# Performance work log

Measured on AMD Instinct MI355X. Metric: run time of the kernel, lower is better.

## Reference

```python
import jax, jax.numpy as jnp
import numpy as np

SMOOTH = 1e-05
N_SCALES = 3
# 3x3 cross-shaped boundary kernel, OIHW layout [1,1,3,3]
_KERNEL = jnp.array([[0., 1., 0.], [1., 1., 1.], [0., 1., 0.]], jnp.float32).reshape(1, 1, 3, 3)


def _nearest_ds(t, h, w):
    """torch F.interpolate mode='nearest': src_idx = floor(dst_idx * in/out)."""
    H, W = t.shape[-2], t.shape[-1]
    ih = (jnp.arange(h) * H) // h
    iw = (jnp.arange(w) * W) // w
    return t[..., ih[:, None], iw[None, :]]


def _boundary_dou(probs, tgt, valid):
    # probs, tgt: [B,N,h,w] float32; valid: [B,N] float32 in {0,1}
    B, N, h, w = probs.shape
    Y = jax.lax.conv_general_dilated(
        tgt.reshape(B * N, 1, h, w), _KERNEL,
        window_strides=(1, 1), padding=[(1, 1), (1, 1)],
        dimension_numbers=('NCHW', 'OIHW', 'NCHW')).reshape(B, N, h, w)
    Y = Y * tgt
    Y = jnp.where(Y == 5.0, 0.0, Y)  # interior pixels zeroed, boundary kept
    C = jnp.sum(Y != 0, axis=(-2, -1)).astype(jnp.float32)   # [B,N] boundary count
    S = jnp.sum(tgt != 0, axis=(-2, -1)).astype(jnp.float32)  # [B,N] fg count
    alpha = 2.0 * (1.0 - (C + SMOOTH) / (S + SMOOTH)) - 1.0
    alpha = jnp.minimum(alpha, 0.8)
    inter = jnp.sum(probs * tgt, axis=(-2, -1))
    y_sum = jnp.sum(tgt * tgt, axis=(-2, -1))
    z_sum = jnp.sum(probs * probs, axis=(-2, -1))
    dou = (z_sum + y_sum - 2.0 * inter + SMOOTH) / (z_sum + y_sum - (1.0 + alpha) * inter + SMOOTH)
    per = jnp.where(S > 0, dou, probs.mean(axis=(-2, -1)))  # empty-target fallback
    cnt = valid.sum()
    return jnp.where(cnt > 0, (per * valid).sum() / cnt, 0.0)


def reference(logits0, logits1, logits2, targets, valid_mask):
    outs = [logits0, logits1, logits2]
    ws = np.array([1.0 / 2.0 ** i for i in range(N_SCALES)])
    ws = ws / ws.sum()  # nnU-Net deep supervision weights
    tgt_full = targets.astype(jnp.float32)
    valid = (valid_mask >= 0.5).astype(jnp.float32)
    loss = jnp.float32(0.0)
    for w_i, out in zip(ws, outs):
        h, w = out.shape[-2], out.shape[-1]
        tgt = _nearest_ds(tgt_full, h, w)
        probs = jax.nn.sigmoid(out.astype(jnp.float32))
        loss = loss + jnp.float32(w_i) * _boundary_dou(probs, tgt, valid)
    return loss


def setup_inputs() -> dict:
    key = jax.random.key(0)
    k0, k1, k2, kt = jax.random.split(key, 4)
    B, N = 8, 4
    return {
        'logits0': jax.random.normal(k0, (B, N, 512, 512), jnp.float32),
        'logits1': jax.random.normal(k1, (B, N, 256, 256), jnp.float32),
        'logits2': jax.random.normal(k2, (B, N, 128, 128), jnp.float32),
        'targets': jax.random.randint(kt, (B, N, 512, 512), 0, 2, jnp.int32),
        'valid_mask': jnp.ones((B, N), jnp.float32),
    }
```

## Files before the change

### kernel.cpp

```cpp
#include <hip/hip_runtime.h>

#define SMOOTH 1e-5f

typedef float floatx4 __attribute__((ext_vector_type(4)));
typedef float floatx2 __attribute__((ext_vector_type(2)));


__device__ __forceinline__ float wave_reduce(float v) {
#pragma unroll
    for (int off = 32; off; off >>= 1) v += __shfl_down(v, off, 64);
    return v;
}

__device__ __forceinline__ float sigmoidf(float x) {
    return 1.f / (1.f + __expf(-x));
}

__device__ __forceinline__ unsigned pack8(int4 a, int4 b) {
    return (unsigned)(a.x != 0)        | ((unsigned)(a.y != 0) << 1) |
           ((unsigned)(a.z != 0) << 2) | ((unsigned)(a.w != 0) << 3) |
           ((unsigned)(b.x != 0) << 4) | ((unsigned)(b.y != 0) << 5) |
           ((unsigned)(b.z != 0) << 6) | ((unsigned)(b.w != 0) << 7);
}
__device__ __forceinline__ unsigned pack4(int4 a, int4 b) {
    return (unsigned)(a.x != 0)        | ((unsigned)(a.z != 0) << 1) |
           ((unsigned)(b.x != 0) << 2) | ((unsigned)(b.z != 0) << 3);
}
__device__ __forceinline__ unsigned pack2(int a, int b) {
    return (unsigned)(a != 0) | ((unsigned)(b != 0) << 1);
}

template<int W>
__device__ __forceinline__ void row_proc(unsigned u, unsigned c, unsigned d,
    const float* pr, int lane, int& cC, int& cS, float& aI, float& aZ, float& aP)
{
    unsigned pv = __shfl_up(c, 1);
    unsigned nx = __shfl_down(c, 1);
    if (lane == 0)  pv = 0;
    if (lane == 63) nx = 0;
    const unsigned M = (1u << W) - 1u;
    unsigned lv = ((c << 1) | ((pv >> (W - 1)) & 1u)) & M;
    unsigned rv = ((c >> 1) | ((nx & 1u) << (W - 1))) & M;
    unsigned inter = c & u & d & lv & rv;
    cS += __popc(c);
    cC += __popc(c & ~inter);
#pragma unroll
    for (int j = 0; j < W; ++j) {
        float pj = pr[j];
        aI += ((c >> j) & 1u) ? pj : 0.f;
        aZ += pj * pj;
        aP += pj;
    }
}

__global__ __launch_bounds__(64) void bdou_reduce(
    const float* __restrict__ l0, const float* __restrict__ l1,
    const float* __restrict__ l2, const int* __restrict__ tgt,
    float* __restrict__ ws)
{
    const int blk  = blockIdx.x;
    const int lane = threadIdx.x;

    int scale, img, strip;
    if (blk < 1024)      { scale = 0; img = blk >> 5; strip = blk & 31; }
    else if (blk < 1536) { int b = blk - 1024; scale = 1; img = b >> 4; strip = b & 15; }
    else                 { int b = blk - 1536; scale = 2; img = b >> 3; strip = b & 7; }

    const int* __restrict__ timg = tgt + (size_t)img * 262144;
    const int y0 = strip * 16;

    int   cC = 0, cS = 0;
    float aI = 0.f, aZ = 0.f, aP = 0.f;

    if (scale == 0) {
        const int*   T = timg + lane * 8;
        const float* L = l0 + (size_t)img * 262144 + lane * 8;
        unsigned b_prev, b_cur, b_next;
        floatx4 lgA, lgB;
        {
            int yp = (y0 > 0) ? y0 - 1 : 0;
            int4 a0 = *(const int4*)(T + (size_t)yp * 512);
            int4 a1 = *(const int4*)(T + (size_t)yp * 512 + 4);
            int4 c0 = *(const int4*)(T + (size_t)y0 * 512);
            int4 c1 = *(const int4*)(T + (size_t)y0 * 512 + 4);
            int4 d0 = *(const int4*)(T + (size_t)(y0 + 1) * 512);
            int4 d1 = *(const int4*)(T + (size_t)(y0 + 1) * 512 + 4);
            lgA = *(const floatx4*)(L + (size_t)y0 * 512);
            lgB = *(const floatx4*)(L + (size_t)y0 * 512 + 4);
            b_prev = pack8(a0, a1); b_cur = pack8(c0, c1); b_next = pack8(d0, d1);
        }
        for (int i = 0; i < 16; ++i) {
            int y   = y0 + i;
            int ypf = (y + 2 < 512) ? y + 2 : 511;
            int ylg = (y + 1 < 512) ? y + 1 : 511;
            int4 p0 = *(const int4*)(T + (size_t)ypf * 512);
            int4 p1 = *(const int4*)(T + (size_t)ypf * 512 + 4);
            floatx4 nA = *(const floatx4*)(L + (size_t)ylg * 512);
            floatx4 nB = *(const floatx4*)(L + (size_t)ylg * 512 + 4);
            unsigned u = (y > 0)   ? b_prev : 0u;
            unsigned d = (y < 511) ? b_next : 0u;
            float pr[8] = {sigmoidf(lgA.x), sigmoidf(lgA.y), sigmoidf(lgA.z), sigmoidf(lgA.w),
                           sigmoidf(lgB.x), sigmoidf(lgB.y), sigmoidf(lgB.z), sigmoidf(lgB.w)};
            row_proc<8>(u, b_cur, d, pr, lane, cC, cS, aI, aZ, aP);
            b_prev = b_cur; b_cur = b_next; b_next = pack8(p0, p1);
            lgA = nA; lgB = nB;
        }
    } else if (scale == 1) {
        const int*   T = timg + lane * 8;
        const float* L = l1 + (size_t)img * 65536 + lane * 4;
        unsigned b_prev, b_cur, b_next;
        floatx4 lgA;
        {
            int yp = (y0 > 0) ? y0 - 1 : 0;
            int4 a0 = *(const int4*)(T + (size_t)(2 * yp) * 512);
            int4 a1 = *(const int4*)(T + (size_t)(2 * yp) * 512 + 4);
            int4 c0 = *(const int4*)(T + (size_t)(2 * y0) * 512);
            int4 c1 = *(const int4*)(T + (size_t)(2 * y0) * 512 + 4);
            int4 d0 = *(const int4*)(T + (size_t)(2 * (y0 + 1)) * 512);
            int4 d1 = *(const int4*)(T + (size_t)(2 * (y0 + 1)) * 512 + 4);
            lgA = *(const floatx4*)(L + (size_t)y0 * 256);
            b_prev = pack4(a0, a1); b_cur = pack4(c0, c1); b_next = pack4(d0, d1);
        }
        for (int i = 0; i < 16; ++i) {
            int y   = y0 + i;
            int ypf = (y + 2 < 256) ? y + 2 : 255;
            int ylg = (y + 1 < 256) ? y + 1 : 255;
            int4 p0 = *(const int4*)(T + (size_t)(2 * ypf) * 512);
            int4 p1 = *(const int4*)(T + (size_t)(2 * ypf) * 512 + 4);
            floatx4 nA = *(const floatx4*)(L + (size_t)ylg * 256);
            unsigned u = (y > 0)   ? b_prev : 0u;
            unsigned d = (y < 255) ? b_next : 0u;
            float pr[4] = {sigmoidf(lgA.x), sigmoidf(lgA.y), sigmoidf(lgA.z), sigmoidf(lgA.w)};
            row_proc<4>(u, b_cur, d, pr, lane, cC, cS, aI, aZ, aP);
            b_prev = b_cur; b_cur = b_next; b_next = pack4(p0, p1);
            lgA = nA;
        }
    } else {
        const int*   T = timg + lane * 8;
        const float* L = l2 + (size_t)img * 16384 + lane * 2;
        unsigned b_prev, b_cur, b_next;
        floatx2 lgA;
        {
            int yp = (y0 > 0) ? y0 - 1 : 0;
            int a0 = T[(size_t)(4 * yp) * 512],       a1 = T[(size_t)(4 * yp) * 512 + 4];
            int c0 = T[(size_t)(4 * y0) * 512],       c1 = T[(size_t)(4 * y0) * 512 + 4];
            int d0 = T[(size_t)(4 * (y0 + 1)) * 512], d1 = T[(size_t)(4 * (y0 + 1)) * 512 + 4];
            lgA = *(const floatx2*)(L + (size_t)y0 * 128);
            b_prev = pack2(a0, a1); b_cur = pack2(c0, c1); b_next = pack2(d0, d1);
        }
        for (int i = 0; i < 16; ++i) {
            int y   = y0 + i;
            int ypf = (y + 2 < 128) ? y + 2 : 127;
            int ylg = (y + 1 < 128) ? y + 1 : 127;
            int p0 = T[(size_t)(4 * ypf) * 512];
            int p1 = T[(size_t)(4 * ypf) * 512 + 4];
            floatx2 nA = *(const floatx2*)(L + (size_t)ylg * 128);
            unsigned u = (y > 0)   ? b_prev : 0u;
            unsigned d = (y < 127) ? b_next : 0u;
            float pr[2] = {sigmoidf(lgA.x), sigmoidf(lgA.y)};
            row_proc<2>(u, b_cur, d, pr, lane, cC, cS, aI, aZ, aP);
            b_prev = b_cur; b_cur = b_next; b_next = pack2(p0, p1);
            lgA = nA;
        }
    }

    float vals[5] = {(float)cC, (float)cS, aI, aZ, aP};
#pragma unroll
    for (int k = 0; k < 5; ++k) vals[k] = wave_reduce(vals[k]);
    if (lane == 0) {
        float* w = ws + (scale * 32 + img) * 5;
        atomicAdd(&w[0], vals[0]);
        atomicAdd(&w[1], vals[1]);
        atomicAdd(&w[2], vals[2]);
        atomicAdd(&w[3], vals[3]);
        atomicAdd(&w[4], vals[4]);
    }
}

__global__ void bdou_final(const float* __restrict__ ws,
                           const float* __restrict__ valid_mask,
                           float* __restrict__ out)
{
    int tid = threadIdx.x;
    float contrib = 0.f, cpart = 0.f;
    if (tid < 96) {
        int s = tid >> 5, i = tid & 31;
        const float* w = ws + tid * 5;
        float C = w[0], S = w[1], I = w[2], Z = w[3], P = w[4];
        float valid = (valid_mask[i] >= 0.5f) ? 1.f : 0.f;
        float alpha = fminf(2.f * (1.f - (C + SMOOTH) / (S + SMOOTH)) - 1.f, 0.8f);
        float dou = (Z + S - 2.f * I + SMOOTH) /
                    (Z + S - (1.f + alpha) * I + SMOOTH);
        const float wts[3]  = {4.f / 7.f, 2.f / 7.f, 1.f / 7.f};
        const float pixc[3] = {262144.f, 65536.f, 16384.f};
        float per = (S > 0.f) ? dou : (P / pixc[s]);
        contrib = wts[s] * per * valid;
        if (tid < 32) cpart = valid;
    }
    contrib = wave_reduce(contrib);
    cpart   = wave_reduce(cpart);
    __shared__ float sm[2][2];
    int wv = tid >> 6, ln = tid & 63;
    if (ln == 0) { sm[wv][0] = contrib; sm[wv][1] = cpart; }
    __syncthreads();
    if (tid == 0) {
        float tot = sm[0][0] + sm[1][0];
        float cnt = sm[0][1] + sm[1][1];
        out[0] = (cnt > 0.f) ? tot / cnt : 0.f;
    }
}

extern "C" void kernel_launch(void* const* d_in, const int* in_sizes, int n_in,
                              void* d_out, int out_size, void* d_ws, size_t ws_size,
                              hipStream_t stream) {
    const float* l0 = (const float*)d_in[0];
    const float* l1 = (const float*)d_in[1];
    const float* l2 = (const float*)d_in[2];
    const int*   tg = (const int*)d_in[3];
    const float* vm = (const float*)d_in[4];
    float* ws = (float*)d_ws;

    (void)hipMemsetAsync(ws, 0, 3 * 32 * 5 * sizeof(float), stream);
    bdou_reduce<<<1792, 64, 0, stream>>>(l0, l1, l2, tg, ws);
    bdou_final<<<1, 128, 0, stream>>>(ws, vm, (float*)d_out);
}
```

Baseline: 125.6 us.

## Split boundary stencil from elementwise reductions into separate block roles

The single fused kernel is split into two kinds of work inside one launch. Most blocks (256 threads each) do flat, vectorized passes over logits and downsampled targets to accumulate foreground count, intersection, squared sum and probability sum. A set of extra blocks runs only the bitpacked cross-stencil boundary count, using two waves per block over 32-row strips. The intent is to raise parallelism and simplify the heavy per-pixel sigmoid path, at the cost of reading the target rows a second time and leaving half the threads idle in the stencil blocks.

```diff
diff --git a/kernel.cpp b/kernel.cpp
--- a/kernel.cpp
+++ b/kernel.cpp
@@ -3,7 +3,6 @@
 #define SMOOTH 1e-5f
 
 typedef float floatx4 __attribute__((ext_vector_type(4)));
-typedef float floatx2 __attribute__((ext_vector_type(2)));
 
 
 __device__ __forceinline__ float wave_reduce(float v) {
@@ -31,8 +30,7 @@
 }
 
 template<int W>
-__device__ __forceinline__ void row_proc(unsigned u, unsigned c, unsigned d,
-    const float* pr, int lane, int& cC, int& cS, float& aI, float& aZ, float& aP)
+__device__ __forceinline__ int stencil_cnt(unsigned u, unsigned c, unsigned d, int lane)
 {
     unsigned pv = __shfl_up(c, 1);
     unsigned nx = __shfl_down(c, 1);
@@ -41,139 +39,174 @@
     const unsigned M = (1u << W) - 1u;
     unsigned lv = ((c << 1) | ((pv >> (W - 1)) & 1u)) & M;
     unsigned rv = ((c >> 1) | ((nx & 1u) << (W - 1))) & M;
-    unsigned inter = c & u & d & lv & rv;
-    cS += __popc(c);
-    cC += __popc(c & ~inter);
-#pragma unroll
-    for (int j = 0; j < W; ++j) {
-        float pj = pr[j];
-        aI += ((c >> j) & 1u) ? pj : 0.f;
-        aZ += pj * pj;
-        aP += pj;
-    }
-}
-
-__global__ __launch_bounds__(64) void bdou_reduce(
+    return __popc(c & ~(u & d & lv & rv));
+}
+
+__global__ __launch_bounds__(256) void bdou_main(
     const float* __restrict__ l0, const float* __restrict__ l1,
     const float* __restrict__ l2, const int* __restrict__ tgt,
     float* __restrict__ ws)
 {
-    const int blk  = blockIdx.x;
-    const int lane = threadIdx.x;
-
-    int scale, img, strip;
-    if (blk < 1024)      { scale = 0; img = blk >> 5; strip = blk & 31; }
-    else if (blk < 1536) { int b = blk - 1024; scale = 1; img = b >> 4; strip = b & 15; }
-    else                 { int b = blk - 1536; scale = 2; img = b >> 3; strip = b & 7; }
-
-    const int* __restrict__ timg = tgt + (size_t)img * 262144;
-    const int y0 = strip * 16;
-
-    int   cC = 0, cS = 0;
-    float aI = 0.f, aZ = 0.f, aP = 0.f;
-
-    if (scale == 0) {
-        const int*   T = timg + lane * 8;
-        const float* L = l0 + (size_t)img * 262144 + lane * 8;
-        unsigned b_prev, b_cur, b_next;
-        floatx4 lgA, lgB;
-        {
-            int yp = (y0 > 0) ? y0 - 1 : 0;
-            int4 a0 = *(const int4*)(T + (size_t)yp * 512);
-            int4 a1 = *(const int4*)(T + (size_t)yp * 512 + 4);
-            int4 c0 = *(const int4*)(T + (size_t)y0 * 512);
-            int4 c1 = *(const int4*)(T + (size_t)y0 * 512 + 4);
-            int4 d0 = *(const int4*)(T + (size_t)(y0 + 1) * 512);
-            int4 d1 = *(const int4*)(T + (size_t)(y0 + 1) * 512 + 4);
-            lgA = *(const floatx4*)(L + (size_t)y0 * 512);
-            lgB = *(const floatx4*)(L + (size_t)y0 * 512 + 4);
-            b_prev = pack8(a0, a1); b_cur = pack8(c0, c1); b_next = pack8(d0, d1);
-        }
-        for (int i = 0; i < 16; ++i) {
-            int y   = y0 + i;
-            int ypf = (y + 2 < 512) ? y + 2 : 511;
-            int ylg = (y + 1 < 512) ? y + 1 : 511;
-            int4 p0 = *(const int4*)(T + (size_t)ypf * 512);
-            int4 p1 = *(const int4*)(T + (size_t)ypf * 512 + 4);
-            floatx4 nA = *(const floatx4*)(L + (size_t)ylg * 512);
-            floatx4 nB = *(const floatx4*)(L + (size_t)ylg * 512 + 4);
-            unsigned u = (y > 0)   ? b_prev : 0u;
-            unsigned d = (y < 511) ? b_next : 0u;
-            float pr[8] = {sigmoidf(lgA.x), sigmoidf(lgA.y), sigmoidf(lgA.z), sigmoidf(lgA.w),
-                           sigmoidf(lgB.x), sigmoidf(lgB.y), sigmoidf(lgB.z), sigmoidf(lgB.w)};
-            row_proc<8>(u, b_cur, d, pr, lane, cC, cS, aI, aZ, aP);
-            b_prev = b_cur; b_cur = b_next; b_next = pack8(p0, p1);
-            lgA = nA; lgB = nB;
-        }
-    } else if (scale == 1) {
-        const int*   T = timg + lane * 8;
-        const float* L = l1 + (size_t)img * 65536 + lane * 4;
-        unsigned b_prev, b_cur, b_next;
-        floatx4 lgA;
-        {
-            int yp = (y0 > 0) ? y0 - 1 : 0;
-            int4 a0 = *(const int4*)(T + (size_t)(2 * yp) * 512);
-            int4 a1 = *(const int4*)(T + (size_t)(2 * yp) * 512 + 4);
-            int4 c0 = *(const int4*)(T + (size_t)(2 * y0) * 512);
-            int4 c1 = *(const int4*)(T + (size_t)(2 * y0) * 512 + 4);
-            int4 d0 = *(const int4*)(T + (size_t)(2 * (y0 + 1)) * 512);
-            int4 d1 = *(const int4*)(T + (size_t)(2 * (y0 + 1)) * 512 + 4);
-            lgA = *(const floatx4*)(L + (size_t)y0 * 256);
-            b_prev = pack4(a0, a1); b_cur = pack4(c0, c1); b_next = pack4(d0, d1);
-        }
-        for (int i = 0; i < 16; ++i) {
-            int y   = y0 + i;
-            int ypf = (y + 2 < 256) ? y + 2 : 255;
-            int ylg = (y + 1 < 256) ? y + 1 : 255;
-            int4 p0 = *(const int4*)(T + (size_t)(2 * ypf) * 512);
-            int4 p1 = *(const int4*)(T + (size_t)(2 * ypf) * 512 + 4);
-            floatx4 nA = *(const floatx4*)(L + (size_t)ylg * 256);
-            unsigned u = (y > 0)   ? b_prev : 0u;
-            unsigned d = (y < 255) ? b_next : 0u;
-            float pr[4] = {sigmoidf(lgA.x), sigmoidf(lgA.y), sigmoidf(lgA.z), sigmoidf(lgA.w)};
-            row_proc<4>(u, b_cur, d, pr, lane, cC, cS, aI, aZ, aP);
-            b_prev = b_cur; b_cur = b_next; b_next = pack4(p0, p1);
-            lgA = nA;
+    const int blk = blockIdx.x;
+    const int tid = threadIdx.x;
+    const int w = tid >> 6, lane = tid & 63;
+
+    if (blk < 1344) {
+        int scale, img, chunk;
+        if (blk < 1024)      { scale = 0; img = blk >> 5; chunk = blk & 31; }
+        else if (blk < 1280) { int b = blk - 1024; scale = 1; img = b >> 3; chunk = b & 7; }
+        else                 { int b = blk - 1280; scale = 2; img = b >> 1; chunk = b & 1; }
+        const int* __restrict__ T = tgt + (size_t)img * 262144;
+        int cS = 0; float aI = 0.f, aZ = 0.f, aP = 0.f;
+        const int qbase = chunk * 2048 + tid;
+
+        if (scale == 0) {
+            const float* __restrict__ L = l0 + (size_t)img * 262144;
+#pragma unroll
+            for (int it = 0; it < 8; ++it) {
+                int p = (qbase + it * 256) * 4;
+                floatx4 lg = *(const floatx4*)(L + p);
+                int4    tv = *(const int4*)(T + p);
+                float pr[4] = {sigmoidf(lg.x), sigmoidf(lg.y), sigmoidf(lg.z), sigmoidf(lg.w)};
+                int   tb[4] = {tv.x != 0, tv.y != 0, tv.z != 0, tv.w != 0};
+#pragma unroll
+                for (int j = 0; j < 4; ++j) {
+                    cS += tb[j];
+                    aI += pr[j] * (float)tb[j];
+                    aZ += pr[j] * pr[j];
+                    aP += pr[j];
+                }
+            }
+        } else if (scale == 1) {
+            const float* __restrict__ L = l1 + (size_t)img * 65536;
+#pragma unroll
+            for (int it = 0; it < 8; ++it) {
+                int p = (qbase + it * 256) * 4;
+                int y = p >> 8, x = p & 255;
+                floatx4 lg = *(const floatx4*)(L + (size_t)y * 256 + x);
+                const int* r = T + (size_t)(2 * y) * 512 + 2 * x;
+                int4 a = *(const int4*)(r);
+                int4 b = *(const int4*)(r + 4);
+                float pr[4] = {sigmoidf(lg.x), sigmoidf(lg.y), sigmoidf(lg.z), sigmoidf(lg.w)};
+                int   tb[4] = {a.x != 0, a.z != 0, b.x != 0, b.z != 0};
+#pragma unroll
+                for (int j = 0; j < 4; ++j) {
+                    cS += tb[j];
+                    aI += pr[j] * (float)tb[j];
+                    aZ += pr[j] * pr[j];
+                    aP += pr[j];
+                }
+            }
+        } else {
+            const float* __restrict__ L = l2 + (size_t)img * 16384;
+#pragma unroll
+            for (int it = 0; it < 8; ++it) {
+                int p = (qbase + it * 256) * 4;
+                int y = p >> 7, x = p & 127;
+                floatx4 lg = *(const floatx4*)(L + (size_t)y * 128 + x);
+                const int* r = T + (size_t)(4 * y) * 512 + 4 * x;
+                int t0 = r[0], t1 = r[4], t2 = r[8], t3 = r[12];
+                float pr[4] = {sigmoidf(lg.x), sigmoidf(lg.y), sigmoidf(lg.z), sigmoidf(lg.w)};
+                int   tb[4] = {t0 != 0, t1 != 0, t2 != 0, t3 != 0};
+#pragma unroll
+                for (int j = 0; j < 4; ++j) {
+                    cS += tb[j];
+                    aI += pr[j] * (float)tb[j];
+                    aZ += pr[j] * pr[j];
+                    aP += pr[j];
+                }
+            }
+        }
+
+        __shared__ float red[4][4];
+        float vals[4] = {(float)cS, aI, aZ, aP};
+#pragma unroll
+        for (int k = 0; k < 4; ++k) vals[k] = wave_reduce(vals[k]);
+        if (lane == 0) {
+#pragma unroll
+            for (int k = 0; k < 4; ++k) red[w][k] = vals[k];
+        }
+        __syncthreads();
+        if (tid < 4) {
+            float s = red[0][tid] + red[1][tid] + red[2][tid] + red[3][tid];
+            atomicAdd(&ws[(scale * 32 + img) * 5 + 1 + tid], s);
         }
     } else {
-        const int*   T = timg + lane * 8;
-        const float* L = l2 + (size_t)img * 16384 + lane * 2;
-        unsigned b_prev, b_cur, b_next;
-        floatx2 lgA;
-        {
-            int yp = (y0 > 0) ? y0 - 1 : 0;
-            int a0 = T[(size_t)(4 * yp) * 512],       a1 = T[(size_t)(4 * yp) * 512 + 4];
-            int c0 = T[(size_t)(4 * y0) * 512],       c1 = T[(size_t)(4 * y0) * 512 + 4];
-            int d0 = T[(size_t)(4 * (y0 + 1)) * 512], d1 = T[(size_t)(4 * (y0 + 1)) * 512 + 4];
-            lgA = *(const floatx2*)(L + (size_t)y0 * 128);
-            b_prev = pack2(a0, a1); b_cur = pack2(c0, c1); b_next = pack2(d0, d1);
-        }
-        for (int i = 0; i < 16; ++i) {
-            int y   = y0 + i;
-            int ypf = (y + 2 < 128) ? y + 2 : 127;
-            int ylg = (y + 1 < 128) ? y + 1 : 127;
-            int p0 = T[(size_t)(4 * ypf) * 512];
-            int p1 = T[(size_t)(4 * ypf) * 512 + 4];
-            floatx2 nA = *(const floatx2*)(L + (size_t)ylg * 128);
-            unsigned u = (y > 0)   ? b_prev : 0u;
-            unsigned d = (y < 127) ? b_next : 0u;
-            float pr[2] = {sigmoidf(lgA.x), sigmoidf(lgA.y)};
-            row_proc<2>(u, b_cur, d, pr, lane, cC, cS, aI, aZ, aP);
-            b_prev = b_cur; b_cur = b_next; b_next = pack2(p0, p1);
-            lgA = nA;
-        }
-    }
-
-    float vals[5] = {(float)cC, (float)cS, aI, aZ, aP};
-#pragma unroll
-    for (int k = 0; k < 5; ++k) vals[k] = wave_reduce(vals[k]);
-    if (lane == 0) {
-        float* w = ws + (scale * 32 + img) * 5;
-        atomicAdd(&w[0], vals[0]);
-        atomicAdd(&w[1], vals[1]);
-        atomicAdd(&w[2], vals[2]);
-        atomicAdd(&w[3], vals[3]);
-        atomicAdd(&w[4], vals[4]);
+        if (w >= 2) return;
+        const int task = (blk - 1344) * 2 + w;
+        int scale, img, strip;
+        if (task < 512)      { scale = 0; img = task >> 4; strip = task & 15; }
+        else if (task < 768) { int b = task - 512; scale = 1; img = b >> 3; strip = b & 7; }
+        else                 { int b = task - 768; scale = 2; img = b >> 2; strip = b & 3; }
+        const int* __restrict__ T = tgt + (size_t)img * 262144 + lane * 8;
+        const int y0 = strip * 32;
+        int cC = 0;
+
+        if (scale == 0) {
+            unsigned rp = 0, rc;
+            if (y0 > 0) {
+                int4 a = *(const int4*)(T + (size_t)(y0 - 1) * 512);
+                int4 b = *(const int4*)(T + (size_t)(y0 - 1) * 512 + 4);
+                rp = pack8(a, b);
+            }
+            {
+                int4 a = *(const int4*)(T + (size_t)y0 * 512);
+                int4 b = *(const int4*)(T + (size_t)y0 * 512 + 4);
+                rc = pack8(a, b);
+            }
+            int4 f0 = *(const int4*)(T + (size_t)(y0 + 1) * 512);
+            int4 f1 = *(const int4*)(T + (size_t)(y0 + 1) * 512 + 4);
+            for (int i = 0; i < 32; ++i) {
+                int y = y0 + i;
+                unsigned rn = (y < 511) ? pack8(f0, f1) : 0u;
+                int yn = (y + 2 <= 511) ? y + 2 : 511;
+                f0 = *(const int4*)(T + (size_t)yn * 512);
+                f1 = *(const int4*)(T + (size_t)yn * 512 + 4);
+                cC += stencil_cnt<8>(rp, rc, rn, lane);
+                rp = rc; rc = rn;
+            }
+        } else if (scale == 1) {
+            unsigned rp = 0, rc;
+            if (y0 > 0) {
+                int4 a = *(const int4*)(T + (size_t)(2 * (y0 - 1)) * 512);
+                int4 b = *(const int4*)(T + (size_t)(2 * (y0 - 1)) * 512 + 4);
+                rp = pack4(a, b);
+            }
+            {
+                int4 a = *(const int4*)(T + (size_t)(2 * y0) * 512);
+                int4 b = *(const int4*)(T + (size_t)(2 * y0) * 512 + 4);
+                rc = pack4(a, b);
+            }
+            int4 f0 = *(const int4*)(T + (size_t)(2 * (y0 + 1)) * 512);
+            int4 f1 = *(const int4*)(T + (size_t)(2 * (y0 + 1)) * 512 + 4);
+            for (int i = 0; i < 32; ++i) {
+                int y = y0 + i;
+                unsigned rn = (y < 255) ? pack4(f0, f1) : 0u;
+                int yn = (y + 2 <= 255) ? y + 2 : 255;
+                f0 = *(const int4*)(T + (size_t)(2 * yn) * 512);
+                f1 = *(const int4*)(T + (size_t)(2 * yn) * 512 + 4);
+                cC += stencil_cnt<4>(rp, rc, rn, lane);
+                rp = rc; rc = rn;
+            }
+        } else {
+            unsigned rp = 0, rc;
+            if (y0 > 0) rp = pack2(T[(size_t)(4 * (y0 - 1)) * 512], T[(size_t)(4 * (y0 - 1)) * 512 + 4]);
+            rc = pack2(T[(size_t)(4 * y0) * 512], T[(size_t)(4 * y0) * 512 + 4]);
+            int f0 = T[(size_t)(4 * (y0 + 1)) * 512];
+            int f1 = T[(size_t)(4 * (y0 + 1)) * 512 + 4];
+            for (int i = 0; i < 32; ++i) {
+                int y = y0 + i;
+                unsigned rn = (y < 127) ? pack2(f0, f1) : 0u;
+                int yn = (y + 2 <= 127) ? y + 2 : 127;
+                f0 = T[(size_t)(4 * yn) * 512];
+                f1 = T[(size_t)(4 * yn) * 512 + 4];
+                cC += stencil_cnt<2>(rp, rc, rn, lane);
+                rp = rc; rc = rn;
+            }
+        }
+
+        float c = wave_reduce((float)cC);
+        if (lane == 0) atomicAdd(&ws[(scale * 32 + img) * 5 + 0], c);
     }
 }
 
@@ -221,6 +254,6 @@
     float* ws = (float*)d_ws;
 
     (void)hipMemsetAsync(ws, 0, 3 * 32 * 5 * sizeof(float), stream);
-    bdou_reduce<<<1792, 64, 0, stream>>>(l0, l1, l2, tg, ws);
+    bdou_main<<<1792, 256, 0, stream>>>(l0, l1, l2, tg, ws);
     bdou_final<<<1, 128, 0, stream>>>(ws, vm, (float*)d_out);
 }
```

New measurement: 127.1 us. About the same (+1.3%).
